# Optimization experiments

Measured on AMD Instinct MI355X. Metric: run time of the kernel, lower is better.

The kernel has to match this reference:

```python
import jax, jax.numpy as jnp
import numpy as np

SIGMA_V = 0.1   # std of topic-level Gaussian noise theta_V
SCALE_R = 0.1   # 'sigma2_R' is used as the Normal scale in the torch code


def setup_inputs() -> dict:
    key = jax.random.key(0)
    ks = jax.random.split(key, 8)
    T, L, NT, KC, D = 20, 2000, 1000, 256, 5
    return {
        "Q": jax.random.normal(ks[0], (NT, 32), dtype=jnp.float32),
        "V": jax.random.normal(ks[1], (NT, KC), dtype=jnp.float32),
        "R": jax.random.uniform(ks[2], (T, L, NT), dtype=jnp.float32),
        "neighbor_weights": jax.random.normal(ks[3], (NT, NT), dtype=jnp.float32),
        "U": jax.random.normal(ks[4], (T, L, KC, D), dtype=jnp.float32),
        "U_emb_w": jax.random.normal(ks[5], (1, D), dtype=jnp.float32),
        "U_emb_b": jax.random.normal(ks[6], (1,), dtype=jnp.float32),
        "noise": jax.random.normal(ks[7], (NT, KC), dtype=jnp.float32),
        "C": jax.random.randint(jax.random.fold_in(key, 9), (T, L, NT), 0, 2, dtype=jnp.int32),
    }


def reference(Q, V, R, neighbor_weights, U, U_emb_w, U_emb_b, noise, C):
    # (nw[:, :, None] * V[None]).sum(0)[b, k] == V[b, k] * nw.sum(0)[b]
    # -> avoid materializing the (nt, nt, kc) intermediate.
    V_j = V * jnp.sum(neighbor_weights, axis=0)[:, None] + SIGMA_V * noise  # (nt, kc)
    # Linear(dim=5 -> 1) applied to U, then squeeze: (T, L, kc)
    U_emb = jnp.einsum('tlkd,d->tlk', U, U_emb_w[0]) + U_emb_b[0]
    # scores[t, i, j] = sigmoid(U_emb[t, i, :] . V_j[j, :])
    mu = jax.nn.sigmoid(jnp.einsum('tlk,jk->tlj', U_emb, V_j))  # (T, L, nt)
    # Normal(mu, SCALE_R).log_prob(R), summed over entries where C == 1
    log_prob = (-0.5 * jnp.square((R - mu) / SCALE_R)
                - jnp.log(SCALE_R) - 0.5 * jnp.log(2.0 * jnp.pi))
    return jnp.sum(jnp.where(C == 1, log_prob, 0.0))
```

## Files before the change

kernel.cpp:

```cpp
#include <hip/hip_runtime.h>
#include <hip/hip_bf16.h>

typedef __attribute__((ext_vector_type(8))) short short8;
typedef __attribute__((ext_vector_type(4))) float f32x4;
typedef __attribute__((ext_vector_type(4))) int   i32x4;
typedef __attribute__((ext_vector_type(4))) unsigned short us4;

#define NTOP 1000
#define KC   256
#define MROWS 40000
#define MBLK  64

static __device__ __forceinline__ unsigned short f2bf(float x) {
    union { float f; unsigned u; } v; v.f = x;
    unsigned r = (v.u + 0x7FFFu + ((v.u >> 16) & 1u)) >> 16;
    return (unsigned short)r;
}

__global__ void k_prep(const float* __restrict__ nw,
                       float* __restrict__ colsum) {
    int j  = blockIdx.x * 256 + threadIdx.x;
    int i0 = blockIdx.y * 8;
    if (j < NTOP) {
        float s = 0.f;
        int iend = min(i0 + 8, NTOP);
        for (int i = i0; i < iend; ++i) s += nw[(size_t)i * NTOP + j];
        atomicAdd(colsum + j, s);
    }
}

__global__ void k_vj(const float* __restrict__ V,
                     const float* __restrict__ noise,
                     const float* __restrict__ colsum,
                     unsigned short* __restrict__ Bp) {
    int t  = blockIdx.x * 256 + threadIdx.x;
    int nt = t >> 9;
    int s  = (t >> 6) & 7;
    int l  = t & 63;
    int lm = l & 15, lq = l >> 4;
    int n  = nt * 16 + lm;
    int k0 = s * 32 + lq * 8;
    union { short8 v; unsigned short us[8]; } pk;
    if (n < NTOP) {
        float cs = colsum[n];
        #pragma unroll
        for (int j = 0; j < 8; ++j) {
            int idx = n * KC + k0 + j;
            pk.us[j] = f2bf(V[idx] * cs + 0.1f * noise[idx]);
        }
    } else {
        #pragma unroll
        for (int j = 0; j < 8; ++j) pk.us[j] = 0;
    }
    reinterpret_cast<short8*>(Bp)[t] = pk.v;
}

__global__ __launch_bounds__(256) void k_cmask(const int* __restrict__ C,
                                               unsigned* __restrict__ Cb) {
    const int idx = blockIdx.x * 256 + threadIdx.x;
    const int m = idx >> 5, w = idx & 31;
    const int* p = C + (size_t)m * NTOP + w * 32;
    const int nbase = w * 32;
    unsigned word = 0;
    if (nbase + 32 <= NTOP) {
        #pragma unroll
        for (int j = 0; j < 32; j += 4) {
            i32x4 c4 = *reinterpret_cast<const i32x4*>(p + j);
            word |= (unsigned)(c4.x == 1) << (j + 0);
            word |= (unsigned)(c4.y == 1) << (j + 1);
            word |= (unsigned)(c4.z == 1) << (j + 2);
            word |= (unsigned)(c4.w == 1) << (j + 3);
        }
    } else {
        for (int j = 0; j < NTOP - nbase; ++j)
            word |= (unsigned)(p[j] == 1) << j;
    }
    Cb[idx] = word;
}

__global__ __launch_bounds__(256, 3) void k_main(
    const float* __restrict__ U, const float* __restrict__ w5,
    const float* __restrict__ b1, const short8* __restrict__ Bf,
    const float* __restrict__ R, const unsigned* __restrict__ Cb,
    float* __restrict__ out)
{
    __shared__ short8 Afrag[4][8][64];
    __shared__ float  rawU[4 * 1284];

    const int tid  = threadIdx.x;
    const int wave = tid >> 6;
    const int l    = tid & 63;
    const int lm = l & 15;
    const int lq = l >> 4;
    const int m0 = blockIdx.x * MBLK;

    const float w0 = w5[0], w1 = w5[1], w2 = w5[2], w3 = w5[3], w4 = w5[4];
    const float bb = b1[0];

    {
        const float* ub = U + (size_t)m0 * (KC * 5);

        float* dst0; float* dst1; float* dst2; float* dst3; float* dst4;
        {
            int i0 = 0 * 1024 + tid * 4; dst0 = &rawU[(i0 / 1280) * 1284 + i0 % 1280];
            int i1 = 1 * 1024 + tid * 4; dst1 = &rawU[(i1 / 1280) * 1284 + i1 % 1280];
            int i2 = 2 * 1024 + tid * 4; dst2 = &rawU[(i2 / 1280) * 1284 + i2 % 1280];
            int i3 = 3 * 1024 + tid * 4; dst3 = &rawU[(i3 / 1280) * 1284 + i3 % 1280];
            int i4 = 4 * 1024 + tid * 4; dst4 = &rawU[(i4 / 1280) * 1284 + i4 % 1280];
        }
        const int chunk = tid >> 1;
        const int half  = tid & 1;
        const int s_c   = chunk >> 4;
        const int lqc   = (chunk >> 2) & 3;
        const int lmh   = chunk & 3;
        const int fi    = lmh * 1284 + s_c * 160 + lqc * 40 + half * 20;

        f32x4 st0, st1, st2, st3, st4;
        st0 = *reinterpret_cast<const f32x4*>(ub + 0 * 1024 + tid * 4);
        st1 = *reinterpret_cast<const f32x4*>(ub + 1 * 1024 + tid * 4);
        st2 = *reinterpret_cast<const f32x4*>(ub + 2 * 1024 + tid * 4);
        st3 = *reinterpret_cast<const f32x4*>(ub + 3 * 1024 + tid * 4);
        st4 = *reinterpret_cast<const f32x4*>(ub + 4 * 1024 + tid * 4);

        for (int g = 0; g < 16; ++g) {
            *reinterpret_cast<f32x4*>(dst0) = st0;
            *reinterpret_cast<f32x4*>(dst1) = st1;
            *reinterpret_cast<f32x4*>(dst2) = st2;
            *reinterpret_cast<f32x4*>(dst3) = st3;
            *reinterpret_cast<f32x4*>(dst4) = st4;
            __syncthreads();

            if (g < 15) {
                const float* src = ub + (size_t)(g + 1) * 5120;
                st0 = *reinterpret_cast<const f32x4*>(src + 0 * 1024 + tid * 4);
                st1 = *reinterpret_cast<const f32x4*>(src + 1 * 1024 + tid * 4);
                st2 = *reinterpret_cast<const f32x4*>(src + 2 * 1024 + tid * 4);
                st3 = *reinterpret_cast<const f32x4*>(src + 3 * 1024 + tid * 4);
                st4 = *reinterpret_cast<const f32x4*>(src + 4 * 1024 + tid * 4);
            }

            {
                float u[20];
                #pragma unroll
                for (int i = 0; i < 5; ++i) {
                    f32x4 t = *reinterpret_cast<const f32x4*>(&rawU[fi + i * 4]);
                    u[i*4+0] = t.x; u[i*4+1] = t.y; u[i*4+2] = t.z; u[i*4+3] = t.w;
                }
                us4 pk;
                #pragma unroll
                for (int j = 0; j < 4; ++j) {
                    float e = u[j*5+0]*w0 + u[j*5+1]*w1 + u[j*5+2]*w2
                            + u[j*5+3]*w3 + u[j*5+4]*w4 + bb;
                    pk[j] = f2bf(e);
                }
                const int mt = g >> 2;
                const int ll = lqc * 16 + ((g & 3) * 4 + lmh);
                *reinterpret_cast<us4*>(
                    reinterpret_cast<unsigned short*>(&Afrag[mt][s_c][ll]) + half * 4) = pk;
            }
            __syncthreads();
        }
    }

    const size_t rb0 = (size_t)(m0 +  0 + lm) * NTOP;
    const size_t rb1 = (size_t)(m0 + 16 + lm) * NTOP;
    const size_t rb2 = (size_t)(m0 + 32 + lm) * NTOP;
    const size_t rb3 = (size_t)(m0 + 48 + lm) * NTOP;
    const size_t cb0 = (size_t)(m0 +  0 + lm) * 32;
    const size_t cb1 = (size_t)(m0 + 16 + lm) * 32;
    const size_t cb2 = (size_t)(m0 + 32 + lm) * 32;
    const size_t cb3 = (size_t)(m0 + 48 + lm) * 32;

    auto LOADIT = [&](int nt16_, f32x4* rv_, unsigned* cw_) {
        const int nst = (nt16_ << 4) + (lq << 2);
        if (nst < NTOP) {
            const int ws = nst >> 5;
            rv_[0] = *reinterpret_cast<const f32x4*>(R + rb0 + nst);
            rv_[1] = *reinterpret_cast<const f32x4*>(R + rb1 + nst);
            rv_[2] = *reinterpret_cast<const f32x4*>(R + rb2 + nst);
            rv_[3] = *reinterpret_cast<const f32x4*>(R + rb3 + nst);
            cw_[0] = Cb[cb0 + ws];
            cw_[1] = Cb[cb1 + ws];
            cw_[2] = Cb[cb2 + ws];
            cw_[3] = Cb[cb3 + ws];
        } else {
            #pragma unroll
            for (int q = 0; q < 4; ++q) {
                rv_[q] = (f32x4){0.f, 0.f, 0.f, 0.f};
                cw_[q] = 0u;
            }
        }
    };

    auto LOADBF = [&](int nt16_, short8* b_) {
        #pragma unroll
        for (int s = 0; s < 8; ++s)
            b_[s] = Bf[((nt16_ * 8 + s) << 6) + l];
    };

    float lpsum = 0.f;
    const int nt0 = wave << 4;

    short8 bfc[8], bfn[8];
    f32x4 rv[4]; unsigned cw[4];
    LOADBF(nt0, bfc);
    LOADIT(nt0, rv, cw);

    for (int it = 0; it < 16; ++it) {
        const int nt16 = nt0 + it;

        __builtin_amdgcn_sched_barrier(0);
        if (it < 15) LOADBF(nt16 + 1, bfn);
        __builtin_amdgcn_sched_barrier(0);

        f32x4 acc[4];
        #pragma unroll
        for (int mt = 0; mt < 4; ++mt) acc[mt] = (f32x4){0.f, 0.f, 0.f, 0.f};

        #pragma unroll
        for (int s = 0; s < 8; ++s) {
            const short8 bfr = bfc[s];
            const short8 a0 = Afrag[0][s][l];
            const short8 a1 = Afrag[1][s][l];
            const short8 a2 = Afrag[2][s][l];
            const short8 a3 = Afrag[3][s][l];
            acc[0] = __builtin_amdgcn_mfma_f32_16x16x32_bf16(bfr, a0, acc[0], 0, 0, 0);
            acc[1] = __builtin_amdgcn_mfma_f32_16x16x32_bf16(bfr, a1, acc[1], 0, 0, 0);
            acc[2] = __builtin_amdgcn_mfma_f32_16x16x32_bf16(bfr, a2, acc[2], 0, 0, 0);
            acc[3] = __builtin_amdgcn_mfma_f32_16x16x32_bf16(bfr, a3, acc[3], 0, 0, 0);
        }

        f32x4 rv2[4]; unsigned cw2[4];

        __builtin_amdgcn_sched_barrier(0);
        if (it < 15) LOADIT(nt16 + 1, rv2, cw2);
        __builtin_amdgcn_sched_barrier(0);

        const int sh = ((nt16 & 1) << 4) + (lq << 2);
        #pragma unroll
        for (int mt = 0; mt < 4; ++mt) {
            const unsigned y = cw[mt] >> sh;
            #pragma unroll
            for (int r = 0; r < 4; ++r) {
                float muv = 1.f / (1.f + __expf(-acc[mt][r]));
                float d   = rv[mt][r] - muv;
                float lp  = -50.f * d * d + 1.3836465597893728f;
                if ((y >> r) & 1u) lpsum += lp;
            }
        }

        if (it < 15) {
            #pragma unroll
            for (int s = 0; s < 8; ++s) bfc[s] = bfn[s];
            rv[0] = rv2[0]; cw[0] = cw2[0];
            rv[1] = rv2[1]; cw[1] = cw2[1];
            rv[2] = rv2[2]; cw[2] = cw2[2];
            rv[3] = rv2[3]; cw[3] = cw2[3];
        }
    }

    #pragma unroll
    for (int off = 32; off > 0; off >>= 1) lpsum += __shfl_down(lpsum, off);
    if (l == 0) atomicAdd(out, lpsum);
}

extern "C" void kernel_launch(void* const* d_in, const int* in_sizes, int n_in,
                              void* d_out, int out_size, void* d_ws, size_t ws_size,
                              hipStream_t stream) {
    const float* V     = (const float*)d_in[1];
    const float* R     = (const float*)d_in[2];
    const float* nw    = (const float*)d_in[3];
    const float* U     = (const float*)d_in[4];
    const float* w5    = (const float*)d_in[5];
    const float* b1    = (const float*)d_in[6];
    const float* noise = (const float*)d_in[7];
    const int*   C     = (const int*)d_in[8];
    float* out = (float*)d_out;

    float*          colsum = (float*)d_ws;
    unsigned short* Bp     = (unsigned short*)((char*)d_ws + 8192);
    unsigned*       Cb     = (unsigned*)((char*)d_ws + 532480);

    hipMemsetAsync(colsum, 0, NTOP * sizeof(float), stream);
    hipMemsetAsync(out, 0, sizeof(float), stream);
    hipLaunchKernelGGL(k_prep, dim3(4, 125), dim3(256), 0, stream, nw, colsum);
    hipLaunchKernelGGL(k_vj, dim3(128), dim3(256), 0, stream,
                       V, noise, colsum, Bp);
    hipLaunchKernelGGL(k_cmask, dim3(5000), dim3(256), 0, stream, C, Cb);
    hipLaunchKernelGGL(k_main, dim3(MROWS / MBLK), dim3(256), 0, stream,
                       U, w5, b1, (const short8*)Bp, R, Cb, out);
}
```

Before: 175.3 us.

## Split U embedding into separate kernel and spread main kernel over N tiles

Adds a k_uemb kernel that computes the U linear projection and writes bf16 MFMA A-fragments to workspace. The main kernel then just copies these fragments into shared memory and runs over a 2D grid that splits the topic dimension in two, with higher occupancy (launch bounds 4) and register double-buffering of B fragments and R/C tiles. The goal is to drop the long per-block U staging prologue and gain parallelism, at the cost of an extra kernel launch and a 20MB intermediate written and read back through global memory. If the workspace is too small, the old fused kernel runs instead.

```diff
diff --git a/kernel.cpp b/kernel.cpp
--- a/kernel.cpp
+++ b/kernel.cpp
@@ -10,6 +10,11 @@
 #define KC   256
 #define MROWS 40000
 #define MBLK  64
+#define OFF_BP  8192
+#define OFF_CB  532480
+#define OFF_AF  5652480
+#define WS_FULL 26132480
+#define WS_CB   5652480
 
 static __device__ __forceinline__ unsigned short f2bf(float x) {
     union { float f; unsigned u; } v; v.f = x;
@@ -78,7 +83,161 @@
     Cb[idx] = word;
 }
 
-__global__ __launch_bounds__(256, 3) void k_main(
+__global__ __launch_bounds__(256) void k_uemb(
+    const float* __restrict__ U, const float* __restrict__ w5,
+    const float* __restrict__ b1, short8* __restrict__ Af)
+{
+    const int o  = blockIdx.x * 256 + threadIdx.x;
+    const int l  = o & 63;
+    const int s  = (o >> 6) & 7;
+    const int mt = o >> 9;
+    const int m  = (mt << 4) + (l & 15);
+    const int k0 = (s << 5) + ((l >> 4) << 3);
+    const float w0 = w5[0], w1 = w5[1], w2 = w5[2], w3 = w5[3], w4 = w5[4];
+    const float bb = b1[0];
+
+    const f32x4* up4 = reinterpret_cast<const f32x4*>(U + ((size_t)m * KC + k0) * 5);
+    float u[40];
+    #pragma unroll
+    for (int i = 0; i < 10; ++i) {
+        f32x4 t = up4[i];
+        u[i*4+0] = t.x; u[i*4+1] = t.y; u[i*4+2] = t.z; u[i*4+3] = t.w;
+    }
+    union { short8 v; unsigned short us[8]; } pk;
+    #pragma unroll
+    for (int j = 0; j < 8; ++j) {
+        float e = u[j*5+0]*w0 + u[j*5+1]*w1 + u[j*5+2]*w2
+                + u[j*5+3]*w3 + u[j*5+4]*w4 + bb;
+        pk.us[j] = f2bf(e);
+    }
+    Af[o] = pk.v;
+}
+
+__global__ __launch_bounds__(256, 4) void k_main(
+    const short8* __restrict__ Af, const short8* __restrict__ Bf,
+    const float* __restrict__ R, const unsigned* __restrict__ Cb,
+    float* __restrict__ out)
+{
+    __shared__ short8 Afrag[4][8][64];
+
+    const int tid  = threadIdx.x;
+    const int wave = tid >> 6;
+    const int l    = tid & 63;
+    const int lm = l & 15;
+    const int lq = l >> 4;
+    const int m0 = blockIdx.x * MBLK;
+
+    {
+        const short8* afp = Af + (size_t)blockIdx.x * 2048;
+        short8* ld = reinterpret_cast<short8*>(Afrag);
+        #pragma unroll
+        for (int i = tid; i < 2048; i += 256) ld[i] = afp[i];
+    }
+    __syncthreads();
+
+    const size_t rb0 = (size_t)(m0 +  0 + lm) * NTOP;
+    const size_t rb1 = (size_t)(m0 + 16 + lm) * NTOP;
+    const size_t rb2 = (size_t)(m0 + 32 + lm) * NTOP;
+    const size_t rb3 = (size_t)(m0 + 48 + lm) * NTOP;
+    const size_t cb0 = (size_t)(m0 +  0 + lm) * 32;
+    const size_t cb1 = (size_t)(m0 + 16 + lm) * 32;
+    const size_t cb2 = (size_t)(m0 + 32 + lm) * 32;
+    const size_t cb3 = (size_t)(m0 + 48 + lm) * 32;
+
+    auto LOADIT = [&](int nt16_, f32x4* rv_, unsigned* cw_) {
+        const int nst = (nt16_ << 4) + (lq << 2);
+        if (nst < NTOP) {
+            const int ws = nst >> 5;
+            rv_[0] = *reinterpret_cast<const f32x4*>(R + rb0 + nst);
+            rv_[1] = *reinterpret_cast<const f32x4*>(R + rb1 + nst);
+            rv_[2] = *reinterpret_cast<const f32x4*>(R + rb2 + nst);
+            rv_[3] = *reinterpret_cast<const f32x4*>(R + rb3 + nst);
+            cw_[0] = Cb[cb0 + ws];
+            cw_[1] = Cb[cb1 + ws];
+            cw_[2] = Cb[cb2 + ws];
+            cw_[3] = Cb[cb3 + ws];
+        } else {
+            #pragma unroll
+            for (int q = 0; q < 4; ++q) {
+                rv_[q] = (f32x4){0.f, 0.f, 0.f, 0.f};
+                cw_[q] = 0u;
+            }
+        }
+    };
+
+    auto LOADBF = [&](int nt16_, short8* b_) {
+        #pragma unroll
+        for (int s = 0; s < 8; ++s)
+            b_[s] = Bf[((nt16_ * 8 + s) << 6) + l];
+    };
+
+    float lpsum = 0.f;
+    const int nt0 = blockIdx.y * 32 + (wave << 3);
+
+    short8 bfc[8], bfn[8];
+    f32x4 rv[4]; unsigned cw[4];
+    LOADBF(nt0, bfc);
+    LOADIT(nt0, rv, cw);
+
+    for (int it = 0; it < 8; ++it) {
+        const int nt16 = nt0 + it;
+
+        __builtin_amdgcn_sched_barrier(0);
+        if (it < 7) LOADBF(nt16 + 1, bfn);
+        __builtin_amdgcn_sched_barrier(0);
+
+        f32x4 acc[4];
+        #pragma unroll
+        for (int mt = 0; mt < 4; ++mt) acc[mt] = (f32x4){0.f, 0.f, 0.f, 0.f};
+
+        #pragma unroll
+        for (int s = 0; s < 8; ++s) {
+            const short8 bfr = bfc[s];
+            const short8 a0 = Afrag[0][s][l];
+            const short8 a1 = Afrag[1][s][l];
+            const short8 a2 = Afrag[2][s][l];
+            const short8 a3 = Afrag[3][s][l];
+            acc[0] = __builtin_amdgcn_mfma_f32_16x16x32_bf16(bfr, a0, acc[0], 0, 0, 0);
+            acc[1] = __builtin_amdgcn_mfma_f32_16x16x32_bf16(bfr, a1, acc[1], 0, 0, 0);
+            acc[2] = __builtin_amdgcn_mfma_f32_16x16x32_bf16(bfr, a2, acc[2], 0, 0, 0);
+            acc[3] = __builtin_amdgcn_mfma_f32_16x16x32_bf16(bfr, a3, acc[3], 0, 0, 0);
+        }
+
+        f32x4 rv2[4]; unsigned cw2[4];
+
+        __builtin_amdgcn_sched_barrier(0);
+        if (it < 7) LOADIT(nt16 + 1, rv2, cw2);
+        __builtin_amdgcn_sched_barrier(0);
+
+        const int sh = ((nt16 & 1) << 4) + (lq << 2);
+        #pragma unroll
+        for (int mt = 0; mt < 4; ++mt) {
+            const unsigned y = cw[mt] >> sh;
+            #pragma unroll
+            for (int r = 0; r < 4; ++r) {
+                float muv = 1.f / (1.f + __expf(-acc[mt][r]));
+                float d   = rv[mt][r] - muv;
+                float lp  = -50.f * d * d + 1.3836465597893728f;
+                if ((y >> r) & 1u) lpsum += lp;
+            }
+        }
+
+        if (it < 7) {
+            #pragma unroll
+            for (int s = 0; s < 8; ++s) bfc[s] = bfn[s];
+            rv[0] = rv2[0]; cw[0] = cw2[0];
+            rv[1] = rv2[1]; cw[1] = cw2[1];
+            rv[2] = rv2[2]; cw[2] = cw2[2];
+            rv[3] = rv2[3]; cw[3] = cw2[3];
+        }
+    }
+
+    #pragma unroll
+    for (int off = 32; off > 0; off >>= 1) lpsum += __shfl_down(lpsum, off);
+    if (l == 0) atomicAdd(out, lpsum);
+}
+
+__global__ __launch_bounds__(256, 3) void k_main_fb(
     const float* __restrict__ U, const float* __restrict__ w5,
     const float* __restrict__ b1, const short8* __restrict__ Bf,
     const float* __restrict__ R, const unsigned* __restrict__ Cb,
@@ -99,7 +258,6 @@
 
     {
         const float* ub = U + (size_t)m0 * (KC * 5);
-
         float* dst0; float* dst1; float* dst2; float* dst3; float* dst4;
         {
             int i0 = 0 * 1024 + tid * 4; dst0 = &rawU[(i0 / 1280) * 1284 + i0 % 1280];
@@ -129,7 +287,6 @@
             *reinterpret_cast<f32x4*>(dst3) = st3;
             *reinterpret_cast<f32x4*>(dst4) = st4;
             __syncthreads();
-
             if (g < 15) {
                 const float* src = ub + (size_t)(g + 1) * 5120;
                 st0 = *reinterpret_cast<const f32x4*>(src + 0 * 1024 + tid * 4);
@@ -138,7 +295,6 @@
                 st3 = *reinterpret_cast<const f32x4*>(src + 3 * 1024 + tid * 4);
                 st4 = *reinterpret_cast<const f32x4*>(src + 4 * 1024 + tid * 4);
             }
-
             {
                 float u[20];
                 #pragma unroll
@@ -278,8 +434,9 @@
     float* out = (float*)d_out;
 
     float*          colsum = (float*)d_ws;
-    unsigned short* Bp     = (unsigned short*)((char*)d_ws + 8192);
-    unsigned*       Cb     = (unsigned*)((char*)d_ws + 532480);
+    unsigned short* Bp     = (unsigned short*)((char*)d_ws + OFF_BP);
+    unsigned*       Cb     = (unsigned*)((char*)d_ws + OFF_CB);
+    short8*         Af     = (short8*)((char*)d_ws + OFF_AF);
 
     hipMemsetAsync(colsum, 0, NTOP * sizeof(float), stream);
     hipMemsetAsync(out, 0, sizeof(float), stream);
@@ -287,6 +444,14 @@
     hipLaunchKernelGGL(k_vj, dim3(128), dim3(256), 0, stream,
                        V, noise, colsum, Bp);
     hipLaunchKernelGGL(k_cmask, dim3(5000), dim3(256), 0, stream, C, Cb);
-    hipLaunchKernelGGL(k_main, dim3(MROWS / MBLK), dim3(256), 0, stream,
-                       U, w5, b1, (const short8*)Bp, R, Cb, out);
-}
+
+    if (ws_size >= (size_t)WS_FULL) {
+        hipLaunchKernelGGL(k_uemb, dim3(5000), dim3(256), 0, stream,
+                           U, w5, b1, Af);
+        hipLaunchKernelGGL(k_main, dim3(MROWS / MBLK, 2), dim3(256), 0, stream,
+                           Af, (const short8*)Bp, R, Cb, out);
+    } else {
+        hipLaunchKernelGGL(k_main_fb, dim3(MROWS / MBLK), dim3(256), 0, stream,
+                           U, w5, b1, (const short8*)Bp, R, Cb, out);
+    }
+}
```

Result: slower. 203.1 us (+15.8%).
